# Kernel optimization log

Hardware: AMD Instinct MI355X
Metric: run time of the kernel (lower is better)

The kernel has to match this reference:

```python
import jax, jax.numpy as jnp
import numpy as np

N = 50000
E = 800000
IN = 128
HID = 32
OUT = 32
H1, H2 = 4, 4
NEG_SLOPE = 0.2


def setup_inputs() -> dict:
    key = jax.random.key(0)
    ks = jax.random.split(key, 12)
    x = jax.random.normal(ks[0], (N, IN), dtype=jnp.float32)
    src = jax.random.randint(ks[1], (E,), 0, N, dtype=jnp.int32)
    dst = jax.random.randint(ks[2], (E,), 0, N, dtype=jnp.int32)
    s = 0.1
    # layer 1: fc (IN -> H1*HID, no bias), attn vectors (H1, HID), bias (H1*HID,)
    W1 = jax.random.normal(ks[3], (IN, H1 * HID), dtype=jnp.float32) * s
    al1 = jax.random.normal(ks[4], (H1, HID), dtype=jnp.float32) * s
    ar1 = jax.random.normal(ks[5], (H1, HID), dtype=jnp.float32) * s
    b1 = jnp.zeros((H1 * HID,), dtype=jnp.float32)
    # layer 2: fc (H1*HID -> H2*OUT, no bias)
    W2 = jax.random.normal(ks[6], (H1 * HID, H2 * OUT), dtype=jnp.float32) * s
    al2 = jax.random.normal(ks[7], (H2, OUT), dtype=jnp.float32) * s
    ar2 = jax.random.normal(ks[8], (H2, OUT), dtype=jnp.float32) * s
    b2 = jnp.zeros((H2 * OUT,), dtype=jnp.float32)
    return {"x": x, "W1": W1, "al1": al1, "ar1": ar1, "b1": b1,
            "W2": W2, "al2": al2, "ar2": ar2, "b2": b2,
            "src": src, "dst": dst}


def _gat_layer(x, W, al, ar, b, src, dst, n, h, d):
    # feat_drop is identity (eval mode)
    feat = (x @ W).reshape(n, h, d)                       # [N,H,D]
    el = jnp.einsum('nhd,hd->nh', feat, al)               # [N,H]
    er = jnp.einsum('nhd,hd->nh', feat, ar)               # [N,H]
    e = jax.nn.leaky_relu(el[src] + er[dst], NEG_SLOPE)   # [E,H] SDDMM
    # edge softmax over incoming edges of each destination node
    emax = jax.ops.segment_max(e, dst, num_segments=n)    # [N,H]
    emax = jnp.where(jnp.isfinite(emax), emax, 0.0)       # guard 0-in-degree
    w = jnp.exp(e - emax[dst])                            # [E,H]
    denom = jax.ops.segment_sum(w, dst, num_segments=n)   # [N,H]
    alpha = w / jnp.maximum(denom[dst], 1e-9)             # [E,H]; attn_drop identity
    # SpMM aggregation
    rst = jax.ops.segment_sum(feat[src] * alpha[:, :, None], dst, num_segments=n)
    # residual: in_feats == h*d for both layers -> DGL uses Identity res_fc
    rst = rst + x.reshape(n, h, d)
    rst = rst + b.reshape(1, h, d)
    return rst


def reference(x, W1, al1, ar1, b1, W2, al2, ar2, b2, src, dst):
    h = _gat_layer(x, W1, al1, ar1, b1, src, dst, N, H1, HID)
    h = jax.nn.elu(h)                                     # layer-1 activation
    h = h.reshape(N, H1 * HID)                            # flatten(1)
    h = _gat_layer(h, W2, al2, ar2, b2, src, dst, N, H2, OUT)
    return h.mean(axis=1)                                 # [N,OUT]
```

## Files before the change

### kernel.cpp

```cpp
#include <hip/hip_runtime.h>
#include <cstdint>
#include <cstddef>

#define NEG_SLOPE 0.2f
#define LOG2E 1.44269504088896340736f

typedef __bf16 bf16x8 __attribute__((ext_vector_type(8)));
typedef float  f32x4  __attribute__((ext_vector_type(4)));

__device__ inline unsigned int bf16pair(float a, float b) {
    unsigned int ua = __float_as_uint(a), ub = __float_as_uint(b);
    ua += 0x7fffu + ((ua >> 16) & 1u);
    ub += 0x7fffu + ((ub >> 16) & 1u);
    return (ua >> 16) | (ub & 0xffff0000u);
}
__device__ inline unsigned short bf16r(float x) {
    unsigned int u = __float_as_uint(x);
    u += 0x7fffu + ((u >> 16) & 1u);
    return (unsigned short)(u >> 16);
}

__global__ __launch_bounds__(256) void wtrans_kernel(
    const float* __restrict__ W1, const float* __restrict__ W2,
    unsigned short* __restrict__ Wt1, unsigned short* __restrict__ Wt2)
{
    __shared__ float tile[64][65];
    const float* W = (blockIdx.x < 4) ? W1 : W2;
    unsigned short* Wt = (blockIdx.x < 4) ? Wt1 : Wt2;
    const int tb = blockIdx.x & 3;
    const int k0 = (tb >> 1) * 64, n0 = (tb & 1) * 64;
    const int c = threadIdx.x & 63, r4 = threadIdx.x >> 6;
#pragma unroll
    for (int i = 0; i < 16; ++i) {
        const int r = i * 4 + r4;
        tile[r][c] = W[(size_t)(k0 + r) * 128 + n0 + c];
    }
    __syncthreads();
#pragma unroll
    for (int i = 0; i < 16; ++i) {
        const int nn = i * 4 + r4;
        Wt[(size_t)(n0 + nn) * 128 + k0 + c] = bf16r(tile[c][nn]);
    }
}

__global__ __launch_bounds__(256, 3) void gemm_attn_kernel(
    const float* __restrict__ X, const unsigned short* __restrict__ Wt,
    const float* __restrict__ al, const float* __restrict__ ar,
    unsigned short* __restrict__ feat16, float* __restrict__ el,
    float* __restrict__ er, int n)
{
    __shared__ unsigned short sX[64][136];
    __shared__ unsigned short sW[128][136];

    const int t = threadIdx.x;
    const int rowbase = blockIdx.x * 64;

#pragma unroll
    for (int i = 0; i < 8; ++i) {
        const int idx = t + 256 * i;
        const int row = idx >> 5;
        const int kq  = (idx & 31) * 4;
        int g = rowbase + row; if (g >= n) g = n - 1;
        const float4 v = *(const float4*)&X[(size_t)g * 128 + kq];
        uint2 pk;
        pk.x = bf16pair(v.x, v.y);
        pk.y = bf16pair(v.z, v.w);
        *(uint2*)&sX[row][kq] = pk;
    }
#pragma unroll
    for (int i = 0; i < 8; ++i) {
        const int idx = t + 256 * i;
        const int row = idx >> 4;
        const int q   = idx & 15;
        *(uint4*)&sW[row][q * 8] = *(const uint4*)&Wt[(size_t)row * 128 + q * 8];
    }
    __syncthreads();

    const int lane = t & 63;
    const int w    = t >> 6;
    const int m    = lane & 15;
    const int g4   = lane >> 4;

    bf16x8 a[4];
#pragma unroll
    for (int ks = 0; ks < 4; ++ks)
        a[ks] = *(const bf16x8*)&sX[w * 16 + m][ks * 32 + g4 * 8];

    float elacc[4][4] = {{0}}, eracc[4][4] = {{0}};
    unsigned short fout[8][4];

#pragma unroll
    for (int ct = 0; ct < 8; ct += 2) {
        f32x4 acc0 = {0.f, 0.f, 0.f, 0.f}, acc1 = {0.f, 0.f, 0.f, 0.f};
        const int n0 = ct * 16 + m, n1 = n0 + 16;
#pragma unroll
        for (int ks = 0; ks < 4; ++ks) {
            const bf16x8 b0 = *(const bf16x8*)&sW[n0][ks * 32 + g4 * 8];
            const bf16x8 b1 = *(const bf16x8*)&sW[n1][ks * 32 + g4 * 8];
            acc0 = __builtin_amdgcn_mfma_f32_16x16x32_bf16(a[ks], b0, acc0, 0, 0, 0);
            acc1 = __builtin_amdgcn_mfma_f32_16x16x32_bf16(a[ks], b1, acc1, 0, 0, 0);
        }
        const int h = ct >> 1;
        const float al0 = al[n0] * LOG2E, ar0 = ar[n0] * LOG2E;
        const float al1 = al[n1] * LOG2E, ar1 = ar[n1] * LOG2E;
#pragma unroll
        for (int r = 0; r < 4; ++r) {
            elacc[r][h] += acc0[r] * al0 + acc1[r] * al1;
            eracc[r][h] += acc0[r] * ar0 + acc1[r] * ar1;
            fout[ct][r]     = bf16r(acc0[r]);
            fout[ct + 1][r] = bf16r(acc1[r]);
        }
    }

    __syncthreads();
#pragma unroll
    for (int ct = 0; ct < 8; ++ct)
#pragma unroll
        for (int r = 0; r < 4; ++r)
            sX[w * 16 + g4 * 4 + r][ct * 16 + m] = fout[ct][r];
    __syncthreads();
    {
        const int row = t >> 2;
        const int q   = t & 3;
        const int g   = rowbase + row;
        if (g < n) {
#pragma unroll
            for (int i = 0; i < 4; ++i) {
                const int c0 = q * 8 + i * 32;
                *(uint4*)&feat16[(size_t)g * 128 + c0] = *(const uint4*)&sX[row][c0];
            }
        }
    }

#pragma unroll
    for (int r = 0; r < 4; ++r)
#pragma unroll
        for (int h = 0; h < 4; ++h) {
            float a_ = elacc[r][h], b_ = eracc[r][h];
            a_ += __shfl_xor(a_, 1); b_ += __shfl_xor(b_, 1);
            a_ += __shfl_xor(a_, 2); b_ += __shfl_xor(b_, 2);
            a_ += __shfl_xor(a_, 4); b_ += __shfl_xor(b_, 4);
            a_ += __shfl_xor(a_, 8); b_ += __shfl_xor(b_, 8);
            elacc[r][h] = a_; eracc[r][h] = b_;
        }
    if (m == 0) {
#pragma unroll
        for (int r = 0; r < 4; ++r) {
            const int row = rowbase + w * 16 + g4 * 4 + r;
            if (row < n) {
#pragma unroll
                for (int h = 0; h < 4; ++h) {
                    el[(size_t)row * 4 + h] = elacc[r][h];
                    er[(size_t)row * 4 + h] = eracc[r][h];
                }
            }
        }
    }
}

__global__ void rank_kernel(const int* __restrict__ dst, int* __restrict__ deg,
                            int* __restrict__ rank, int E)
{
    const int e4 = (blockIdx.x * blockDim.x + threadIdx.x) * 4;
    if (e4 + 4 <= E) {
        const int4 d = *(const int4*)&dst[e4];
        int4 r;
        r.x = atomicAdd(&deg[d.x], 1);
        r.y = atomicAdd(&deg[d.y], 1);
        r.z = atomicAdd(&deg[d.z], 1);
        r.w = atomicAdd(&deg[d.w], 1);
        *(int4*)&rank[e4] = r;
    } else {
        for (int e = e4; e < E; ++e) rank[e] = atomicAdd(&deg[dst[e]], 1);
    }
}

__global__ __launch_bounds__(1024) void scan_kernel(
    const int* __restrict__ deg, int* __restrict__ off, int n)
{
    __shared__ int wsums[16];
    __shared__ int s_carry;
    const int tid  = threadIdx.x;
    const int lane = tid & 63;
    const int wid  = tid >> 6;

    if (tid == 0) { s_carry = 0; off[0] = 0; }
    __syncthreads();

    const int n4 = n >> 2;
    const int4* __restrict__ deg4 = (const int4*)deg;

    for (int base = 0; base < n4; base += 1024) {
        const int i4 = base + tid;
        int4 v = make_int4(0, 0, 0, 0);
        if (i4 < n4) v = deg4[i4];
        const int t0 = v.x, t1 = t0 + v.y, t2 = t1 + v.z, t3 = t2 + v.w;

        int x = t3;
#pragma unroll
        for (int d = 1; d < 64; d <<= 1) {
            int y = __shfl_up(x, d);
            if (lane >= d) x += y;
        }
        if (lane == 63) wsums[wid] = x;
        __syncthreads();

        if (wid == 0 && lane < 16) {
            int xx = wsums[lane];
#pragma unroll
            for (int d = 1; d < 16; d <<= 1) {
                int y = __shfl_up(xx, d);
                if (lane >= d) xx += y;
            }
            wsums[lane] = xx;
        }
        __syncthreads();

        const int wp   = (wid == 0) ? 0 : wsums[wid - 1];
        const int excl = s_carry + wp + (x - t3);
        if (i4 < n4) {
            off[4 * i4 + 1] = excl + t0;
            off[4 * i4 + 2] = excl + t1;
            off[4 * i4 + 3] = excl + t2;
            off[4 * i4 + 4] = excl + t3;
        }
        __syncthreads();
        if (tid == 0) s_carry += wsums[15];
        __syncthreads();
    }
}

__global__ void place_kernel(const int* __restrict__ src, const int* __restrict__ dst,
                             const int* __restrict__ off, const int* __restrict__ rank,
                             int* __restrict__ csr_src, int E)
{
    const int e4 = (blockIdx.x * blockDim.x + threadIdx.x) * 4;
    if (e4 + 4 <= E) {
        const int4 s = *(const int4*)&src[e4];
        const int4 d = *(const int4*)&dst[e4];
        const int4 r = *(const int4*)&rank[e4];
        const int o0 = off[d.x], o1 = off[d.y], o2 = off[d.z], o3 = off[d.w];
        csr_src[o0 + r.x] = s.x;
        csr_src[o1 + r.y] = s.y;
        csr_src[o2 + r.z] = s.z;
        csr_src[o3 + r.w] = s.w;
    } else {
        for (int e = e4; e < E; ++e)
            csr_src[off[dst[e]] + rank[e]] = src[e];
    }
}

template <bool LAYER2>
__global__ __launch_bounds__(256) void agg_kernel(
    const int* __restrict__ off, const int* __restrict__ csr_src,
    const unsigned short* __restrict__ feat16, const float* __restrict__ el,
    const float* __restrict__ er, const float* __restrict__ resid,
    const float* __restrict__ bias, float* __restrict__ out, int n)
{
    const int lane = threadIdx.x & 63;
    const int node = blockIdx.x * 4 + (threadIdx.x >> 6);
    if (node >= n) return;

    const int hh = lane >> 5;
    const int q  = lane & 31;
    const int h  = q >> 3;

    const float erh = er[node * 4 + h];
    const uint2* __restrict__ fb2 = (const uint2*)feat16;

    const int beg = off[node], end = off[node + 1];

    float a0 = 0.f, a1 = 0.f, a2 = 0.f, a3 = 0.f, sw = 0.f;

    int j = beg;
    for (; j + 4 <= end; j += 4) {
        const int sA = csr_src[j + hh];
        const int sB = csr_src[j + 2 + hh];
        const float eA = el[sA * 4 + h];
        const float eB = el[sB * 4 + h];
        const uint2 uA = fb2[sA * 32 + q];
        const uint2 uB = fb2[sB * 32 + q];
        float tA = eA + erh; tA = fmaxf(tA, NEG_SLOPE * tA);
        float tB = eB + erh; tB = fmaxf(tB, NEG_SLOPE * tB);
        const float wA = __builtin_amdgcn_exp2f(tA);
        const float wB = __builtin_amdgcn_exp2f(tB);
        a0 += wA * __uint_as_float(uA.x << 16);
        a1 += wA * __uint_as_float(uA.x & 0xffff0000u);
        a2 += wA * __uint_as_float(uA.y << 16);
        a3 += wA * __uint_as_float(uA.y & 0xffff0000u);
        a0 += wB * __uint_as_float(uB.x << 16);
        a1 += wB * __uint_as_float(uB.x & 0xffff0000u);
        a2 += wB * __uint_as_float(uB.y << 16);
        a3 += wB * __uint_as_float(uB.y & 0xffff0000u);
        sw += wA + wB;
    }
    for (; j < end; j += 2) {
        const int jj = j + hh;
        const bool vld = jj < end;
        const int s = csr_src[vld ? jj : j];
        const float e = el[s * 4 + h];
        const uint2 u = fb2[s * 32 + q];
        float t = e + erh; t = fmaxf(t, NEG_SLOPE * t);
        const float w = vld ? __builtin_amdgcn_exp2f(t) : 0.f;
        a0 += w * __uint_as_float(u.x << 16);
        a1 += w * __uint_as_float(u.x & 0xffff0000u);
        a2 += w * __uint_as_float(u.y << 16);
        a3 += w * __uint_as_float(u.y & 0xffff0000u);
        sw += w;
    }

    a0 += __shfl_xor(a0, 32);
    a1 += __shfl_xor(a1, 32);
    a2 += __shfl_xor(a2, 32);
    a3 += __shfl_xor(a3, 32);
    sw += __shfl_xor(sw, 32);

    const float inv = 1.f / fmaxf(sw, 1e-9f);
    const float4 rs = *(const float4*)&resid[node * 128 + q * 4];
    const float4 bs = *(const float4*)&bias[q * 4];
    float v0 = a0 * inv + rs.x + bs.x;
    float v1 = a1 * inv + rs.y + bs.y;
    float v2 = a2 * inv + rs.z + bs.z;
    float v3 = a3 * inv + rs.w + bs.w;

    if (!LAYER2) {
        if (lane < 32) {
            v0 = (v0 > 0.f) ? v0 : expm1f(v0);
            v1 = (v1 > 0.f) ? v1 : expm1f(v1);
            v2 = (v2 > 0.f) ? v2 : expm1f(v2);
            v3 = (v3 > 0.f) ? v3 : expm1f(v3);
            *(float4*)&out[node * 128 + q * 4] = make_float4(v0, v1, v2, v3);
        }
    } else {
        v0 += __shfl_xor(v0, 8);  v1 += __shfl_xor(v1, 8);
        v2 += __shfl_xor(v2, 8);  v3 += __shfl_xor(v3, 8);
        v0 += __shfl_xor(v0, 16); v1 += __shfl_xor(v1, 16);
        v2 += __shfl_xor(v2, 16); v3 += __shfl_xor(v3, 16);
        if (lane < 8)
            *(float4*)&out[node * 32 + q * 4] =
                make_float4(v0 * 0.25f, v1 * 0.25f, v2 * 0.25f, v3 * 0.25f);
    }
}

extern "C" void kernel_launch(void* const* d_in, const int* in_sizes, int n_in,
                              void* d_out, int out_size, void* d_ws, size_t ws_size,
                              hipStream_t stream)
{
    const float* x   = (const float*)d_in[0];
    const float* W1  = (const float*)d_in[1];
    const float* al1 = (const float*)d_in[2];
    const float* ar1 = (const float*)d_in[3];
    const float* b1  = (const float*)d_in[4];
    const float* W2  = (const float*)d_in[5];
    const float* al2 = (const float*)d_in[6];
    const float* ar2 = (const float*)d_in[7];
    const float* b2  = (const float*)d_in[8];
    const int*   src = (const int*)d_in[9];
    const int*   dst = (const int*)d_in[10];

    const int n = in_sizes[0] / 128;
    const int E = in_sizes[9];
    float* out = (float*)d_out;

    char* p = (char*)d_ws;
    float* h1    = (float*)p;          p += (size_t)n * 128 * sizeof(float);
    unsigned short* feat16 = (unsigned short*)p; p += (size_t)n * 128 * sizeof(unsigned short);
    float* el    = (float*)p;          p += (size_t)n * 4 * sizeof(float);
    float* er    = (float*)p;          p += (size_t)n * 4 * sizeof(float);
    int* off     = (int*)p;            p += (size_t)(n + 1) * sizeof(int);
    int* deg     = (int*)p;            p += (size_t)n * sizeof(int);
    int* rank    = (int*)p;            p += (size_t)E * sizeof(int);
    int* csr     = (int*)p;            p += (size_t)E * sizeof(int);
    unsigned short* wt1 = (unsigned short*)p; p += (size_t)128 * 128 * sizeof(unsigned short);
    unsigned short* wt2 = (unsigned short*)p; p += (size_t)128 * 128 * sizeof(unsigned short);

    hipMemsetAsync(deg, 0, (size_t)n * sizeof(int), stream);

    const int gemm_grid  = (n + 63) / 64;
    const int edge4_grid = (E / 4 + 255) / 256;
    const int agg_grid   = (n + 3) / 4;

    wtrans_kernel<<<8, 256, 0, stream>>>(W1, W2, wt1, wt2);
    gemm_attn_kernel<<<gemm_grid, 256, 0, stream>>>(x, wt1, al1, ar1, feat16, el, er, n);
    rank_kernel<<<edge4_grid, 256, 0, stream>>>(dst, deg, rank, E);
    scan_kernel<<<1, 1024, 0, stream>>>(deg, off, n);
    place_kernel<<<edge4_grid, 256, 0, stream>>>(src, dst, off, rank, csr, E);
    agg_kernel<false><<<agg_grid, 256, 0, stream>>>(off, csr, feat16, el, er, x, b1, h1, n);
    gemm_attn_kernel<<<gemm_grid, 256, 0, stream>>>(h1, wt2, al2, ar2, feat16, el, er, n);
    agg_kernel<true><<<agg_grid, 256, 0, stream>>>(off, csr, feat16, el, er, h1, b2, out, n);
}
```

Before: 275.9 us.

## Parallelize degree scan across blocks and use persistent unrolled aggregation kernel

Replaces the single-block serial degree scan with a two-pass multi-block scan over 64 chunks. The aggregation kernel becomes grid-stride over a fixed 2048-block grid and unrolls the edge loop to eight edges per iteration to raise memory-level parallelism. ELU now uses the hardware exp2 instruction instead of expm1f. The scan assumes chunk <= 256 (n up to about 65k) and the exp2-based ELU loses some precision near zero.

```diff
diff --git a/kernel.cpp b/kernel.cpp
--- a/kernel.cpp
+++ b/kernel.cpp
@@ -175,58 +175,72 @@
     }
 }
 
-__global__ __launch_bounds__(1024) void scan_kernel(
-    const int* __restrict__ deg, int* __restrict__ off, int n)
-{
-    __shared__ int wsums[16];
-    __shared__ int s_carry;
-    const int tid  = threadIdx.x;
-    const int lane = tid & 63;
-    const int wid  = tid >> 6;
-
-    if (tid == 0) { s_carry = 0; off[0] = 0; }
-    __syncthreads();
-
-    const int n4 = n >> 2;
-    const int4* __restrict__ deg4 = (const int4*)deg;
-
-    for (int base = 0; base < n4; base += 1024) {
-        const int i4 = base + tid;
-        int4 v = make_int4(0, 0, 0, 0);
-        if (i4 < n4) v = deg4[i4];
-        const int t0 = v.x, t1 = t0 + v.y, t2 = t1 + v.z, t3 = t2 + v.w;
-
-        int x = t3;
+__global__ __launch_bounds__(256) void scan1_kernel(
+    const int* __restrict__ deg, int* __restrict__ off,
+    int* __restrict__ btot, int n4, int chunk)
+{
+    __shared__ int ws[4];
+    const int c    = blockIdx.x;
+    const int t    = threadIdx.x;
+    const int lane = t & 63;
+    const int wid  = t >> 6;
+    const int i4   = c * chunk + t;
+
+    int4 v = make_int4(0, 0, 0, 0);
+    if (t < chunk && i4 < n4) v = ((const int4*)deg)[i4];
+    const int t0 = v.x, t1 = t0 + v.y, t2 = t1 + v.z, t3 = t2 + v.w;
+
+    int x = t3;
+#pragma unroll
+    for (int d = 1; d < 64; d <<= 1) {
+        int y = __shfl_up(x, d);
+        if (lane >= d) x += y;
+    }
+    if (lane == 63) ws[wid] = x;
+    __syncthreads();
+
+    int wbase = 0;
+#pragma unroll
+    for (int k = 0; k < 3; ++k)
+        if (wid > k) wbase += ws[k];
+
+    const int excl = wbase + x - t3;
+    if (t < chunk && i4 < n4) {
+        off[4 * i4 + 1] = excl + t0;
+        off[4 * i4 + 2] = excl + t1;
+        off[4 * i4 + 3] = excl + t2;
+        off[4 * i4 + 4] = excl + t3;
+    }
+    if (t == 255) btot[c] = wbase + x;
+}
+
+__global__ __launch_bounds__(256) void scan2_kernel(
+    const int* __restrict__ btot, int* __restrict__ off, int n4, int chunk)
+{
+    __shared__ int s_base;
+    const int c = blockIdx.x;
+    const int t = threadIdx.x;
+
+    if (t < 64) {
+        const int v = btot[t];
+        int x = v;
 #pragma unroll
         for (int d = 1; d < 64; d <<= 1) {
             int y = __shfl_up(x, d);
-            if (lane >= d) x += y;
-        }
-        if (lane == 63) wsums[wid] = x;
-        __syncthreads();
-
-        if (wid == 0 && lane < 16) {
-            int xx = wsums[lane];
-#pragma unroll
-            for (int d = 1; d < 16; d <<= 1) {
-                int y = __shfl_up(xx, d);
-                if (lane >= d) xx += y;
-            }
-            wsums[lane] = xx;
-        }
-        __syncthreads();
-
-        const int wp   = (wid == 0) ? 0 : wsums[wid - 1];
-        const int excl = s_carry + wp + (x - t3);
-        if (i4 < n4) {
-            off[4 * i4 + 1] = excl + t0;
-            off[4 * i4 + 2] = excl + t1;
-            off[4 * i4 + 3] = excl + t2;
-            off[4 * i4 + 4] = excl + t3;
-        }
-        __syncthreads();
-        if (tid == 0) s_carry += wsums[15];
-        __syncthreads();
+            if ((t & 63) >= d) x += y;
+        }
+        if (t == c) s_base = x - v;
+    }
+    __syncthreads();
+    const int base = s_base;
+
+    if (c == 0 && t == 0) off[0] = 0;
+    const int i4 = c * chunk + t;
+    if (t < chunk && i4 < n4) {
+        off[4 * i4 + 1] += base;
+        off[4 * i4 + 2] += base;
+        off[4 * i4 + 3] += base;
+        off[4 * i4 + 4] += base;
     }
 }
 
@@ -258,87 +272,127 @@
     const float* __restrict__ bias, float* __restrict__ out, int n)
 {
     const int lane = threadIdx.x & 63;
-    const int node = blockIdx.x * 4 + (threadIdx.x >> 6);
-    if (node >= n) return;
-
     const int hh = lane >> 5;
     const int q  = lane & 31;
     const int h  = q >> 3;
 
-    const float erh = er[node * 4 + h];
     const uint2* __restrict__ fb2 = (const uint2*)feat16;
-
-    const int beg = off[node], end = off[node + 1];
-
-    float a0 = 0.f, a1 = 0.f, a2 = 0.f, a3 = 0.f, sw = 0.f;
-
-    int j = beg;
-    for (; j + 4 <= end; j += 4) {
-        const int sA = csr_src[j + hh];
-        const int sB = csr_src[j + 2 + hh];
-        const float eA = el[sA * 4 + h];
-        const float eB = el[sB * 4 + h];
-        const uint2 uA = fb2[sA * 32 + q];
-        const uint2 uB = fb2[sB * 32 + q];
-        float tA = eA + erh; tA = fmaxf(tA, NEG_SLOPE * tA);
-        float tB = eB + erh; tB = fmaxf(tB, NEG_SLOPE * tB);
-        const float wA = __builtin_amdgcn_exp2f(tA);
-        const float wB = __builtin_amdgcn_exp2f(tB);
-        a0 += wA * __uint_as_float(uA.x << 16);
-        a1 += wA * __uint_as_float(uA.x & 0xffff0000u);
-        a2 += wA * __uint_as_float(uA.y << 16);
-        a3 += wA * __uint_as_float(uA.y & 0xffff0000u);
-        a0 += wB * __uint_as_float(uB.x << 16);
-        a1 += wB * __uint_as_float(uB.x & 0xffff0000u);
-        a2 += wB * __uint_as_float(uB.y << 16);
-        a3 += wB * __uint_as_float(uB.y & 0xffff0000u);
-        sw += wA + wB;
-    }
-    for (; j < end; j += 2) {
-        const int jj = j + hh;
-        const bool vld = jj < end;
-        const int s = csr_src[vld ? jj : j];
-        const float e = el[s * 4 + h];
-        const uint2 u = fb2[s * 32 + q];
-        float t = e + erh; t = fmaxf(t, NEG_SLOPE * t);
-        const float w = vld ? __builtin_amdgcn_exp2f(t) : 0.f;
-        a0 += w * __uint_as_float(u.x << 16);
-        a1 += w * __uint_as_float(u.x & 0xffff0000u);
-        a2 += w * __uint_as_float(u.y << 16);
-        a3 += w * __uint_as_float(u.y & 0xffff0000u);
-        sw += w;
-    }
-
-    a0 += __shfl_xor(a0, 32);
-    a1 += __shfl_xor(a1, 32);
-    a2 += __shfl_xor(a2, 32);
-    a3 += __shfl_xor(a3, 32);
-    sw += __shfl_xor(sw, 32);
-
-    const float inv = 1.f / fmaxf(sw, 1e-9f);
-    const float4 rs = *(const float4*)&resid[node * 128 + q * 4];
     const float4 bs = *(const float4*)&bias[q * 4];
-    float v0 = a0 * inv + rs.x + bs.x;
-    float v1 = a1 * inv + rs.y + bs.y;
-    float v2 = a2 * inv + rs.z + bs.z;
-    float v3 = a3 * inv + rs.w + bs.w;
-
-    if (!LAYER2) {
-        if (lane < 32) {
-            v0 = (v0 > 0.f) ? v0 : expm1f(v0);
-            v1 = (v1 > 0.f) ? v1 : expm1f(v1);
-            v2 = (v2 > 0.f) ? v2 : expm1f(v2);
-            v3 = (v3 > 0.f) ? v3 : expm1f(v3);
-            *(float4*)&out[node * 128 + q * 4] = make_float4(v0, v1, v2, v3);
-        }
-    } else {
-        v0 += __shfl_xor(v0, 8);  v1 += __shfl_xor(v1, 8);
-        v2 += __shfl_xor(v2, 8);  v3 += __shfl_xor(v3, 8);
-        v0 += __shfl_xor(v0, 16); v1 += __shfl_xor(v1, 16);
-        v2 += __shfl_xor(v2, 16); v3 += __shfl_xor(v3, 16);
-        if (lane < 8)
-            *(float4*)&out[node * 32 + q * 4] =
-                make_float4(v0 * 0.25f, v1 * 0.25f, v2 * 0.25f, v3 * 0.25f);
+
+    const int nw = gridDim.x << 2;
+    for (int node = blockIdx.x * 4 + (threadIdx.x >> 6); node < n; node += nw) {
+
+        const int beg = off[node], end = off[node + 1];
+        const float erh = er[node * 4 + h];
+
+        float a0 = 0.f, a1 = 0.f, a2 = 0.f, a3 = 0.f, sw = 0.f;
+        int j = beg;
+
+        for (; j + 8 <= end; j += 8) {
+            const int sA = csr_src[j + hh];
+            const int sB = csr_src[j + 2 + hh];
+            const int sC = csr_src[j + 4 + hh];
+            const int sD = csr_src[j + 6 + hh];
+            const float eA = el[sA * 4 + h];
+            const float eB = el[sB * 4 + h];
+            const float eC = el[sC * 4 + h];
+            const float eD = el[sD * 4 + h];
+            const uint2 uA = fb2[sA * 32 + q];
+            const uint2 uB = fb2[sB * 32 + q];
+            const uint2 uC = fb2[sC * 32 + q];
+            const uint2 uD = fb2[sD * 32 + q];
+            float tA = eA + erh; tA = fmaxf(tA, NEG_SLOPE * tA);
+            float tB = eB + erh; tB = fmaxf(tB, NEG_SLOPE * tB);
+            float tC = eC + erh; tC = fmaxf(tC, NEG_SLOPE * tC);
+            float tD = eD + erh; tD = fmaxf(tD, NEG_SLOPE * tD);
+            const float wA = __builtin_amdgcn_exp2f(tA);
+            const float wB = __builtin_amdgcn_exp2f(tB);
+            const float wC = __builtin_amdgcn_exp2f(tC);
+            const float wD = __builtin_amdgcn_exp2f(tD);
+            a0 += wA * __uint_as_float(uA.x << 16);
+            a1 += wA * __uint_as_float(uA.x & 0xffff0000u);
+            a2 += wA * __uint_as_float(uA.y << 16);
+            a3 += wA * __uint_as_float(uA.y & 0xffff0000u);
+            a0 += wB * __uint_as_float(uB.x << 16);
+            a1 += wB * __uint_as_float(uB.x & 0xffff0000u);
+            a2 += wB * __uint_as_float(uB.y << 16);
+            a3 += wB * __uint_as_float(uB.y & 0xffff0000u);
+            a0 += wC * __uint_as_float(uC.x << 16);
+            a1 += wC * __uint_as_float(uC.x & 0xffff0000u);
+            a2 += wC * __uint_as_float(uC.y << 16);
+            a3 += wC * __uint_as_float(uC.y & 0xffff0000u);
+            a0 += wD * __uint_as_float(uD.x << 16);
+            a1 += wD * __uint_as_float(uD.x & 0xffff0000u);
+            a2 += wD * __uint_as_float(uD.y << 16);
+            a3 += wD * __uint_as_float(uD.y & 0xffff0000u);
+            sw += wA + wB + wC + wD;
+        }
+        for (; j + 4 <= end; j += 4) {
+            const int sA = csr_src[j + hh];
+            const int sB = csr_src[j + 2 + hh];
+            const float eA = el[sA * 4 + h];
+            const float eB = el[sB * 4 + h];
+            const uint2 uA = fb2[sA * 32 + q];
+            const uint2 uB = fb2[sB * 32 + q];
+            float tA = eA + erh; tA = fmaxf(tA, NEG_SLOPE * tA);
+            float tB = eB + erh; tB = fmaxf(tB, NEG_SLOPE * tB);
+            const float wA = __builtin_amdgcn_exp2f(tA);
+            const float wB = __builtin_amdgcn_exp2f(tB);
+            a0 += wA * __uint_as_float(uA.x << 16);
+            a1 += wA * __uint_as_float(uA.x & 0xffff0000u);
+            a2 += wA * __uint_as_float(uA.y << 16);
+            a3 += wA * __uint_as_float(uA.y & 0xffff0000u);
+            a0 += wB * __uint_as_float(uB.x << 16);
+            a1 += wB * __uint_as_float(uB.x & 0xffff0000u);
+            a2 += wB * __uint_as_float(uB.y << 16);
+            a3 += wB * __uint_as_float(uB.y & 0xffff0000u);
+            sw += wA + wB;
+        }
+        for (; j < end; j += 2) {
+            const int jj = j + hh;
+            const bool vld = jj < end;
+            const int s = csr_src[vld ? jj : j];
+            const float e = el[s * 4 + h];
+            const uint2 u = fb2[s * 32 + q];
+            float tt = e + erh; tt = fmaxf(tt, NEG_SLOPE * tt);
+            const float w = vld ? __builtin_amdgcn_exp2f(tt) : 0.f;
+            a0 += w * __uint_as_float(u.x << 16);
+            a1 += w * __uint_as_float(u.x & 0xffff0000u);
+            a2 += w * __uint_as_float(u.y << 16);
+            a3 += w * __uint_as_float(u.y & 0xffff0000u);
+            sw += w;
+        }
+
+        float c0 = a0 + __shfl_xor(a0, 32);
+        float c1 = a1 + __shfl_xor(a1, 32);
+        float c2 = a2 + __shfl_xor(a2, 32);
+        float c3 = a3 + __shfl_xor(a3, 32);
+        float cw = sw + __shfl_xor(sw, 32);
+
+        const float inv = 1.f / fmaxf(cw, 1e-9f);
+        const float4 rs = *(const float4*)&resid[node * 128 + q * 4];
+        float v0 = c0 * inv + rs.x + bs.x;
+        float v1 = c1 * inv + rs.y + bs.y;
+        float v2 = c2 * inv + rs.z + bs.z;
+        float v3 = c3 * inv + rs.w + bs.w;
+
+        if (!LAYER2) {
+            if (lane < 32) {
+                v0 = (v0 > 0.f) ? v0 : (__builtin_amdgcn_exp2f(v0 * LOG2E) - 1.f);
+                v1 = (v1 > 0.f) ? v1 : (__builtin_amdgcn_exp2f(v1 * LOG2E) - 1.f);
+                v2 = (v2 > 0.f) ? v2 : (__builtin_amdgcn_exp2f(v2 * LOG2E) - 1.f);
+                v3 = (v3 > 0.f) ? v3 : (__builtin_amdgcn_exp2f(v3 * LOG2E) - 1.f);
+                *(float4*)&out[node * 128 + q * 4] = make_float4(v0, v1, v2, v3);
+            }
+        } else {
+            v0 += __shfl_xor(v0, 8);  v1 += __shfl_xor(v1, 8);
+            v2 += __shfl_xor(v2, 8);  v3 += __shfl_xor(v3, 8);
+            v0 += __shfl_xor(v0, 16); v1 += __shfl_xor(v1, 16);
+            v2 += __shfl_xor(v2, 16); v3 += __shfl_xor(v3, 16);
+            if (lane < 8)
+                *(float4*)&out[node * 32 + q * 4] =
+                    make_float4(v0 * 0.25f, v1 * 0.25f, v2 * 0.25f, v3 * 0.25f);
+        }
     }
 }
 
@@ -373,17 +427,21 @@
     int* csr     = (int*)p;            p += (size_t)E * sizeof(int);
     unsigned short* wt1 = (unsigned short*)p; p += (size_t)128 * 128 * sizeof(unsigned short);
     unsigned short* wt2 = (unsigned short*)p; p += (size_t)128 * 128 * sizeof(unsigned short);
+    int* btot    = (int*)p;            p += 64 * sizeof(int);
 
     hipMemsetAsync(deg, 0, (size_t)n * sizeof(int), stream);
 
+    const int n4 = n >> 2;
+    const int chunk = (n4 + 63) >> 6;
     const int gemm_grid  = (n + 63) / 64;
     const int edge4_grid = (E / 4 + 255) / 256;
-    const int agg_grid   = (n + 3) / 4;
+    const int agg_grid   = 2048;
 
     wtrans_kernel<<<8, 256, 0, stream>>>(W1, W2, wt1, wt2);
     gemm_attn_kernel<<<gemm_grid, 256, 0, stream>>>(x, wt1, al1, ar1, feat16, el, er, n);
     rank_kernel<<<edge4_grid, 256, 0, stream>>>(dst, deg, rank, E);
-    scan_kernel<<<1, 1024, 0, stream>>>(deg, off, n);
+    scan1_kernel<<<64, 256, 0, stream>>>(deg, off, btot, n4, chunk);
+    scan2_kernel<<<64, 256, 0, stream>>>(btot, off, n4, chunk);
     place_kernel<<<edge4_grid, 256, 0, stream>>>(src, dst, off, rank, csr, E);
     agg_kernel<false><<<agg_grid, 256, 0, stream>>>(off, csr, feat16, el, er, x, b1, h1, n);
     gemm_attn_kernel<<<gemm_grid, 256, 0, stream>>>(h1, wt2, al2, ar2, feat16, el, er, n);
```

New measurement: 254.3 us. 7.8% less time.
